# Kernel tuning notes

Hardware: AMD Instinct MI355X
Metric: run time of the kernel (lower is better)

## Reference

```python
import jax, jax.numpy as jnp
import numpy as np

B, T, H, S = 2, 2048, 16, 64
E = H * S  # 1024

def layernorm(x, w, b, eps=1e-5):
    mu = jnp.mean(x, axis=-1, keepdims=True)
    var = jnp.mean((x - mu) ** 2, axis=-1, keepdims=True)
    return (x - mu) * jax.lax.rsqrt(var + eps) * w + b

def setup_inputs() -> dict:
    key = jax.random.key(0)
    ks = jax.random.split(key, 12)
    w = lambda k, shape: (0.02 * jax.random.normal(k, shape)).astype(jnp.float32)
    return {
        "x": jax.random.normal(ks[0], (B, T, E), dtype=jnp.float32),
        "prev": jax.random.normal(ks[1], (B, T, T, H), dtype=jnp.float32),
        "kqv_w": w(ks[2], (3 * S, S)),      # torch Linear weight [out,in], no bias
        "proj_w": w(ks[3], (E, E)),
        "ln1_w": jnp.ones((E,), jnp.float32),
        "ln1_b": jnp.zeros((E,), jnp.float32),
        "ln2_w": jnp.ones((E,), jnp.float32),
        "ln2_b": jnp.zeros((E,), jnp.float32),
        "ff_w1": w(ks[4], (4 * E, E)),
        "ff_b1": jnp.zeros((4 * E,), jnp.float32),
        "ff_w2": w(ks[5], (E, 4 * E)),
        "ff_b2": jnp.zeros((E,), jnp.float32),
    }

def reference(x, prev, kqv_w, proj_w, ln1_w, ln1_b, ln2_w, ln2_b, ff_w1, ff_b1, ff_w2, ff_b2):
    b, t, _ = x.shape
    xh = x.reshape(b, t, H, S)                       # [B,T,H,S]
    kqv = jnp.einsum('bths,os->btho', xh, kqv_w)     # [B,T,H,3S]
    k, q, v = jnp.split(kqv, 3, axis=-1)             # split order: k,q,v
    att_score = jnp.einsum('bihk,bjhk->bijh', q, k) / jnp.sqrt(jnp.float32(S)) + prev
    att = jax.nn.softmax(att_score, axis=2)          # softmax over j (keys)
    res = jnp.einsum('btih,bihs->bths', att, v).reshape(b, t, E)
    mha = res @ proj_w.T                             # proj, dropout=0
    x1 = layernorm(x + mha, ln1_w, ln1_b)
    ff = jax.nn.gelu(x1 @ ff_w1.T + ff_b1, approximate=False) @ ff_w2.T + ff_b2
    x2 = layernorm(x1 + ff, ln2_w, ln2_b)
    return x2, att_score
```

## Files before the change

kernel.cpp:

```cpp
#include <hip/hip_runtime.h>
#include <hip/hip_bf16.h>
#include <math.h>

#define Bd 2
#define Td 2048
#define Hd 16
#define Sd 64
#define Ed 1024
#define Fd 4096

typedef __attribute__((ext_vector_type(8))) short short8;
typedef __attribute__((ext_vector_type(4))) float f32x4;
typedef __hip_bfloat16 bf16;

__device__ __forceinline__ unsigned short f2bfu(float f){
  bf16 h = __float2bfloat16(f);
  unsigned short u;
  __builtin_memcpy(&u, &h, 2);
  return u;
}

__global__ __launch_bounds__(256) void cvt_bf16_kernel(const float* __restrict__ src,
                                                       bf16* __restrict__ dst, int n4){
  int i = blockIdx.x*256 + threadIdx.x;
  int stride = gridDim.x*256;
  for (; i < n4; i += stride){
    float4 v = ((const float4*)src)[i];
    bf16* d = dst + (size_t)i*4;
    d[0] = __float2bfloat16(v.x);
    d[1] = __float2bfloat16(v.y);
    d[2] = __float2bfloat16(v.z);
    d[3] = __float2bfloat16(v.w);
  }
}

__global__ __launch_bounds__(192) void kqv_kernel(const float* __restrict__ x, const float* __restrict__ w,
    bf16* __restrict__ kb, bf16* __restrict__ qb, bf16* __restrict__ vb){
  __shared__ float xs[Ed];
  int bt = blockIdx.x;
  int o = threadIdx.x;
  const float* xrow = x + (size_t)bt*Ed;
  for (int i = o; i < Ed; i += 192) xs[i] = xrow[i];
  __syncthreads();
  float4 wr[16];
  const float4* w4 = (const float4*)(w + o*Sd);
  #pragma unroll
  for (int i = 0; i < 16; i++) wr[i] = w4[i];
  int part = o >> 6, sidx = o & 63;
  bf16* ob = (part == 0) ? kb : (part == 1 ? qb : vb);
  ob += (size_t)bt*Hd*Sd + sidx;
  for (int h = 0; h < Hd; h++){
    const float4* xh4 = (const float4*)(xs + h*Sd);
    float a0=0.f,a1=0.f,a2=0.f,a3=0.f;
    #pragma unroll
    for (int i = 0; i < 16; i++){
      float4 xv = xh4[i];
      a0 = fmaf(xv.x, wr[i].x, a0);
      a1 = fmaf(xv.y, wr[i].y, a1);
      a2 = fmaf(xv.z, wr[i].z, a2);
      a3 = fmaf(xv.w, wr[i].w, a3);
    }
    ob[h*Sd] = __float2bfloat16((a0+a1)+(a2+a3));
  }
}

__global__ __launch_bounds__(256) void vt_kernel(const bf16* __restrict__ vb, bf16* __restrict__ vt){
  __shared__ bf16 tile[64][72];
  int t0 = blockIdx.x*64, h = blockIdx.y, b = blockIdx.z;
  int tid = threadIdx.x;
  for (int i = tid; i < 4096; i += 256){
    int tt = i >> 6, s = i & 63;
    tile[tt][s] = vb[(((size_t)b*Td + t0 + tt)*Hd + h)*Sd + s];
  }
  __syncthreads();
  for (int i = tid; i < 4096; i += 256){
    int s = i >> 6, tt = i & 63;
    vt[(((size_t)b*Hd + h)*Sd + s)*Td + t0 + tt] = tile[tt][s];
  }
}

__global__ __launch_bounds__(1024) void attn_score_kernel(
    const bf16* __restrict__ qb, const bf16* __restrict__ kb,
    const float* __restrict__ prev, float* __restrict__ att,
    float* __restrict__ m_ws, float* __restrict__ linv_ws){
  int i0 = blockIdx.x*16, b = blockIdx.y;
  int tid = threadIdx.x;
  int wid = tid >> 6, lane = tid & 63, col = lane & 15, quad = lane >> 4;
  __shared__ float Ss[16][16][17];
  __shared__ float Mp[4][16][16];
  __shared__ float Lp[4][16][16];

  const bf16* qbase = qb + (((size_t)b*Td + i0 + col)*Hd + wid)*Sd + quad*8;
  short8 aq0 = *(const short8*)(qbase);
  short8 aq1 = *(const short8*)(qbase + 32);

  int ii = tid >> 6, jq = (tid >> 4) & 3, h2 = tid & 15;
  float m_t = -1e30f, l_t = 0.f;

  for (int jt = 0; jt < Td/16; jt++){
    int j0 = jt*16;
    const bf16* kbase = kb + (((size_t)b*Td + j0 + col)*Hd + wid)*Sd + quad*8;
    short8 bk0 = *(const short8*)(kbase);
    short8 bk1 = *(const short8*)(kbase + 32);
    f32x4 acc = {0.f, 0.f, 0.f, 0.f};
    acc = __builtin_amdgcn_mfma_f32_16x16x32_bf16(aq0, bk0, acc, 0, 0, 0);
    acc = __builtin_amdgcn_mfma_f32_16x16x32_bf16(aq1, bk1, acc, 0, 0, 0);
    #pragma unroll
    for (int r = 0; r < 4; r++) Ss[wid][quad*4 + r][col] = acc[r];
    __syncthreads();
    {
      size_t gb = (((size_t)b*Td + i0 + ii)*Td + j0 + jq*4)*Hd + h2;
      float v0 = Ss[h2][ii][jq*4+0]*0.125f + prev[gb];
      float v1 = Ss[h2][ii][jq*4+1]*0.125f + prev[gb + Hd];
      float v2 = Ss[h2][ii][jq*4+2]*0.125f + prev[gb + 2*Hd];
      float v3 = Ss[h2][ii][jq*4+3]*0.125f + prev[gb + 3*Hd];
      att[gb]        = v0;
      att[gb + Hd]   = v1;
      att[gb + 2*Hd] = v2;
      att[gb + 3*Hd] = v3;
      float mx = fmaxf(fmaxf(v0, v1), fmaxf(v2, v3));
      float nm = fmaxf(m_t, mx);
      float sc = __expf(m_t - nm);
      l_t = l_t*sc + __expf(v0-nm) + __expf(v1-nm) + __expf(v2-nm) + __expf(v3-nm);
      m_t = nm;
    }
    __syncthreads();
  }
  Mp[jq][ii][h2] = m_t;
  Lp[jq][ii][h2] = l_t;
  __syncthreads();
  if (jq == 0){
    float m0 = Mp[0][ii][h2], m1 = Mp[1][ii][h2], m2 = Mp[2][ii][h2], m3 = Mp[3][ii][h2];
    float M = fmaxf(fmaxf(m0, m1), fmaxf(m2, m3));
    float L = Lp[0][ii][h2]*__expf(m0-M) + Lp[1][ii][h2]*__expf(m1-M)
            + Lp[2][ii][h2]*__expf(m2-M) + Lp[3][ii][h2]*__expf(m3-M);
    size_t sidx = ((size_t)b*Td + i0 + ii)*Hd + h2;
    m_ws[sidx] = M;
    linv_ws[sidx] = 1.0f / L;
  }
}

__global__ __launch_bounds__(1024) void attn_av_kernel(
    const float* __restrict__ att, const bf16* __restrict__ vt,
    const float* __restrict__ m_ws, const float* __restrict__ linv_ws,
    bf16* __restrict__ resb){
  int i0 = blockIdx.x*16, b = blockIdx.y;
  int tid = threadIdx.x;
  int wid = tid >> 6, lane = tid & 63, col = lane & 15, quad = lane >> 4;
  __shared__ __align__(16) bf16 Ps[16][17][40];
  __shared__ float Msh[16][16], Lsh[16][16];
  if (tid < 256){
    int ri = tid >> 4, rh = tid & 15;
    size_t sidx = ((size_t)b*Td + i0 + ri)*Hd + rh;
    Msh[ri][rh] = m_ws[sidx];
    Lsh[ri][rh] = linv_ws[sidx];
  }
  __syncthreads();
  f32x4 O[4];
  #pragma unroll
  for (int st = 0; st < 4; st++) O[st] = (f32x4){0.f,0.f,0.f,0.f};

  int cii = tid >> 6, co = (tid >> 4) & 3, ch = tid & 15;
  float mrow = Msh[cii][ch];
  const bf16* vbase = vt + (((size_t)b*Hd + wid)*Sd + col)*Td;

  for (int jt = 0; jt < Td/32; jt++){
    int j0 = jt*32;
    size_t gb = (((size_t)b*Td + i0 + cii)*Td + j0 + co*8)*Hd + ch;
    short8 sv;
    #pragma unroll
    for (int e = 0; e < 8; e++){
      sv[e] = (short)f2bfu(__expf(att[gb + (size_t)e*Hd] - mrow));
    }
    *(short8*)(&Ps[ch][cii][co*8]) = sv;
    __syncthreads();
    short8 a = *(const short8*)(&Ps[wid][col][quad*8]);
    #pragma unroll
    for (int st = 0; st < 4; st++){
      short8 bv = *(const short8*)(vbase + (size_t)st*16*Td + j0 + quad*8);
      O[st] = __builtin_amdgcn_mfma_f32_16x16x32_bf16(a, bv, O[st], 0, 0, 0);
    }
    __syncthreads();
  }
  #pragma unroll
  for (int st = 0; st < 4; st++){
    #pragma unroll
    for (int r = 0; r < 4; r++){
      int irow = quad*4 + r;
      float val = O[st][r] * Lsh[irow][wid];
      resb[((size_t)b*Td + i0 + irow)*Ed + wid*Sd + st*16 + col] = __float2bfloat16(val);
    }
  }
}

template<int EPI>
__global__ __launch_bounds__(256) void gemm_kernel(
    const bf16* __restrict__ A, const bf16* __restrict__ Bw,
    int M, int N, int K,
    const float* __restrict__ bias, const float* __restrict__ addend,
    float* __restrict__ outf, bf16* __restrict__ outb){
  __shared__ __align__(16) bf16 As[128*32];
  __shared__ __align__(16) bf16 Bs[128*32];
  int tid = threadIdx.x;
  int wid = tid >> 6, lane = tid & 63, col = lane & 15, quad = lane >> 4;
  int n0 = blockIdx.x*128, m0 = blockIdx.y*128;
  int wy = wid >> 1, wx = wid & 1;
  f32x4 acc[4][4];
  #pragma unroll
  for (int i = 0; i < 4; i++)
    #pragma unroll
    for (int j = 0; j < 4; j++) acc[i][j] = (f32x4){0.f,0.f,0.f,0.f};

  int srow = tid >> 2, skc = tid & 3;
  for (int k0 = 0; k0 < K; k0 += 32){
    __syncthreads();
    #pragma unroll
    for (int i = 0; i < 2; i++){
      const bf16* gpa = A + (size_t)(m0 + srow + i*64)*K + k0 + skc*8;
      bf16* lpa = As + ((size_t)i*256 + wid*64)*8;
      __builtin_amdgcn_global_load_lds((const __attribute__((address_space(1))) unsigned int*)gpa,
                                       (__attribute__((address_space(3))) unsigned int*)lpa, 16, 0, 0);
      const bf16* gpb = Bw + (size_t)(n0 + srow + i*64)*K + k0 + skc*8;
      bf16* lpb = Bs + ((size_t)i*256 + wid*64)*8;
      __builtin_amdgcn_global_load_lds((const __attribute__((address_space(1))) unsigned int*)gpb,
                                       (__attribute__((address_space(3))) unsigned int*)lpb, 16, 0, 0);
    }
    __syncthreads();
    short8 af[4], bf_[4];
    #pragma unroll
    for (int t = 0; t < 4; t++){
      af[t]  = *(const short8*)(As + (wy*64 + t*16 + col)*32 + quad*8);
      bf_[t] = *(const short8*)(Bs + (wx*64 + t*16 + col)*32 + quad*8);
    }
    #pragma unroll
    for (int i = 0; i < 4; i++)
      #pragma unroll
      for (int j = 0; j < 4; j++)
        acc[i][j] = __builtin_amdgcn_mfma_f32_16x16x32_bf16(af[i], bf_[j], acc[i][j], 0, 0, 0);
  }
  #pragma unroll
  for (int i = 0; i < 4; i++){
    #pragma unroll
    for (int r = 0; r < 4; r++){
      int mrow = m0 + wy*64 + i*16 + quad*4 + r;
      #pragma unroll
      for (int j = 0; j < 4; j++){
        int ncol = n0 + wx*64 + j*16 + col;
        float v = acc[i][j][r];
        size_t oidx = (size_t)mrow*N + ncol;
        if (EPI == 0){
          outf[oidx] = v + addend[oidx];
        } else if (EPI == 1){
          float t = v + bias[ncol];
          outb[oidx] = __float2bfloat16(0.5f*t*(1.0f + erff(t*0.70710678118f)));
        } else {
          outf[oidx] = v + bias[ncol] + addend[oidx];
        }
      }
    }
  }
}

__global__ __launch_bounds__(256) void ln_kernel(const float* __restrict__ in,
    const float* __restrict__ gw, const float* __restrict__ gb,
    float* __restrict__ outf, bf16* __restrict__ outb){
  int row = blockIdx.x, tid = threadIdx.x;
  const float4* r4 = (const float4*)(in + (size_t)row*Ed);
  float4 xv = r4[tid];
  float s  = xv.x + xv.y + xv.z + xv.w;
  float ss = xv.x*xv.x + xv.y*xv.y + xv.z*xv.z + xv.w*xv.w;
  #pragma unroll
  for (int off = 32; off > 0; off >>= 1){
    s  += __shfl_down(s, off);
    ss += __shfl_down(ss, off);
  }
  __shared__ float sb[4], ssb[4], mv[2];
  int lane = tid & 63, wv = tid >> 6;
  if (lane == 0){ sb[wv] = s; ssb[wv] = ss; }
  __syncthreads();
  if (tid == 0){
    float S  = sb[0]+sb[1]+sb[2]+sb[3];
    float SS = ssb[0]+ssb[1]+ssb[2]+ssb[3];
    float mean = S*(1.0f/Ed);
    float var  = SS*(1.0f/Ed) - mean*mean;
    mv[0] = mean; mv[1] = rsqrtf(var + 1e-5f);
  }
  __syncthreads();
  float mean = mv[0], rstd = mv[1];
  float4 wv4 = ((const float4*)gw)[tid];
  float4 bv4 = ((const float4*)gb)[tid];
  float4 o;
  o.x = (xv.x - mean)*rstd*wv4.x + bv4.x;
  o.y = (xv.y - mean)*rstd*wv4.y + bv4.y;
  o.z = (xv.z - mean)*rstd*wv4.z + bv4.z;
  o.w = (xv.w - mean)*rstd*wv4.w + bv4.w;
  if (outf) ((float4*)(outf + (size_t)row*Ed))[tid] = o;
  if (outb){
    bf16* ob = outb + (size_t)row*Ed + tid*4;
    ob[0] = __float2bfloat16(o.x);
    ob[1] = __float2bfloat16(o.y);
    ob[2] = __float2bfloat16(o.z);
    ob[3] = __float2bfloat16(o.w);
  }
}

extern "C" void kernel_launch(void* const* d_in, const int* in_sizes, int n_in,
                              void* d_out, int out_size, void* d_ws, size_t ws_size,
                              hipStream_t stream){
  (void)in_sizes; (void)n_in; (void)out_size; (void)ws_size;
  const float* x      = (const float*)d_in[0];
  const float* prev   = (const float*)d_in[1];
  const float* kqv_w  = (const float*)d_in[2];
  const float* proj_w = (const float*)d_in[3];
  const float* ln1_w  = (const float*)d_in[4];
  const float* ln1_b  = (const float*)d_in[5];
  const float* ln2_w  = (const float*)d_in[6];
  const float* ln2_b  = (const float*)d_in[7];
  const float* ff_w1  = (const float*)d_in[8];
  const float* ff_b1  = (const float*)d_in[9];
  const float* ff_w2  = (const float*)d_in[10];
  const float* ff_b2  = (const float*)d_in[11];

  float* out_x2  = (float*)d_out;
  float* out_att = out_x2 + (size_t)Bd*Td*Ed;

  char* wsp = (char*)d_ws;
  auto alloc = [&](size_t bytes)->char*{
    char* p = wsp;
    wsp += (bytes + 255) & ~(size_t)255;
    return p;
  };
  const size_t NTOK = (size_t)Bd*Td;
  bf16* kb    = (bf16*)alloc(NTOK*Ed*2);
  bf16* qb    = (bf16*)alloc(NTOK*Ed*2);
  bf16* vb    = (bf16*)alloc(NTOK*Ed*2);
  bf16* vtb   = (bf16*)alloc(NTOK*Ed*2);
  bf16* resb  = (bf16*)alloc(NTOK*Ed*2);
  bf16* x1b   = (bf16*)alloc(NTOK*Ed*2);
  bf16* hidb  = (bf16*)alloc(NTOK*Fd*2);
  bf16* pwb   = (bf16*)alloc((size_t)Ed*Ed*2);
  bf16* w1b   = (bf16*)alloc((size_t)Fd*Ed*2);
  bf16* w2b   = (bf16*)alloc((size_t)Ed*Fd*2);
  float* m_ws    = (float*)alloc(NTOK*Hd*4);
  float* linv_ws = (float*)alloc(NTOK*Hd*4);
  float* sum_ws  = (float*)alloc(NTOK*Ed*4);
  float* x1f     = (float*)alloc(NTOK*Ed*4);

  cvt_bf16_kernel<<<1024, 256, 0, stream>>>(proj_w, pwb, (Ed*Ed)/4);
  cvt_bf16_kernel<<<4096, 256, 0, stream>>>(ff_w1, w1b, (Fd*Ed)/4);
  cvt_bf16_kernel<<<4096, 256, 0, stream>>>(ff_w2, w2b, (Ed*Fd)/4);

  kqv_kernel<<<Bd*Td, 192, 0, stream>>>(x, kqv_w, kb, qb, vb);
  vt_kernel<<<dim3(Td/64, Hd, Bd), 256, 0, stream>>>(vb, vtb);

  attn_score_kernel<<<dim3(Td/16, Bd), 1024, 0, stream>>>(qb, kb, prev, out_att, m_ws, linv_ws);
  attn_av_kernel<<<dim3(Td/16, Bd), 1024, 0, stream>>>(out_att, vtb, m_ws, linv_ws, resb);

  gemm_kernel<0><<<dim3(Ed/128, (Bd*Td)/128), 256, 0, stream>>>(
      resb, pwb, Bd*Td, Ed, Ed, nullptr, x, sum_ws, nullptr);
  ln_kernel<<<Bd*Td, 256, 0, stream>>>(sum_ws, ln1_w, ln1_b, x1f, x1b);
  gemm_kernel<1><<<dim3(Fd/128, (Bd*Td)/128), 256, 0, stream>>>(
      x1b, w1b, Bd*Td, Fd, Ed, ff_b1, nullptr, nullptr, hidb);
  gemm_kernel<2><<<dim3(Ed/128, (Bd*Td)/128), 256, 0, stream>>>(
      hidb, w2b, Bd*Td, Ed, Fd, ff_b2, x1f, sum_ws, nullptr);
  ln_kernel<<<Bd*Td, 256, 0, stream>>>(sum_ws, ln2_w, ln2_b, out_x2, nullptr);
}
```

Before: 1.727 ms.

## Fuse attention score and AV kernels into one online-softmax pass

Merges the score kernel and the AV kernel into one kernel that computes scores, writes att_score, and accumulates P·V with an online softmax that rescales the output accumulators. This removes the second full read of the large att tensor from global memory and the m/linv workspace round trip. It also prefetches the next K and prev tiles, processes 32 keys per iteration, and replaces __syncthreads with a custom LDS-wait barrier. In exchange it uses more registers and does extra rescaling work in every iteration.

```diff
diff --git a/kernel.cpp b/kernel.cpp
--- a/kernel.cpp
+++ b/kernel.cpp
@@ -18,6 +18,12 @@
   unsigned short u;
   __builtin_memcpy(&u, &h, 2);
   return u;
+}
+
+__device__ __forceinline__ void bar_lds(){
+  asm volatile("s_waitcnt lgkmcnt(0)" ::: "memory");
+  __builtin_amdgcn_s_barrier();
+  asm volatile("" ::: "memory");
 }
 
 __global__ __launch_bounds__(256) void cvt_bf16_kernel(const float* __restrict__ src,
@@ -79,117 +85,134 @@
   }
 }
 
-__global__ __launch_bounds__(1024) void attn_score_kernel(
+__global__ __launch_bounds__(1024) void attn_fused_kernel(
     const bf16* __restrict__ qb, const bf16* __restrict__ kb,
-    const float* __restrict__ prev, float* __restrict__ att,
-    float* __restrict__ m_ws, float* __restrict__ linv_ws){
+    const bf16* __restrict__ vtp, const float* __restrict__ prev,
+    float* __restrict__ att, bf16* __restrict__ resb){
+  constexpr int NT = Td/32;
   int i0 = blockIdx.x*16, b = blockIdx.y;
   int tid = threadIdx.x;
   int wid = tid >> 6, lane = tid & 63, col = lane & 15, quad = lane >> 4;
-  __shared__ float Ss[16][16][17];
-  __shared__ float Mp[4][16][16];
-  __shared__ float Lp[4][16][16];
+  __shared__ float Ss[16][17][33];
+  __shared__ __align__(16) bf16 Ps[16][17][40];
+  __shared__ float Msc[16][16];
+  __shared__ float Linv[16][16];
 
   const bf16* qbase = qb + (((size_t)b*Td + i0 + col)*Hd + wid)*Sd + quad*8;
   short8 aq0 = *(const short8*)(qbase);
   short8 aq1 = *(const short8*)(qbase + 32);
 
-  int ii = tid >> 6, jq = (tid >> 4) & 3, h2 = tid & 15;
+  int ii = wid, co = (tid >> 4) & 3, h2 = tid & 15;
   float m_t = -1e30f, l_t = 0.f;
 
-  for (int jt = 0; jt < Td/16; jt++){
-    int j0 = jt*16;
-    const bf16* kbase = kb + (((size_t)b*Td + j0 + col)*Hd + wid)*Sd + quad*8;
-    short8 bk0 = *(const short8*)(kbase);
-    short8 bk1 = *(const short8*)(kbase + 32);
-    f32x4 acc = {0.f, 0.f, 0.f, 0.f};
-    acc = __builtin_amdgcn_mfma_f32_16x16x32_bf16(aq0, bk0, acc, 0, 0, 0);
-    acc = __builtin_amdgcn_mfma_f32_16x16x32_bf16(aq1, bk1, acc, 0, 0, 0);
-    #pragma unroll
-    for (int r = 0; r < 4; r++) Ss[wid][quad*4 + r][col] = acc[r];
-    __syncthreads();
+  const bf16* vbase = vtp + (((size_t)b*Hd + wid)*Sd + col)*Td;
+  const bf16* kb0 = kb + (((size_t)b*Td + col)*Hd + wid)*Sd + quad*8;
+  const size_t KJ = (size_t)Hd*Sd;
+
+  short8 kc0 = *(const short8*)(kb0);
+  short8 kc1 = *(const short8*)(kb0 + 32);
+  short8 kc2 = *(const short8*)(kb0 + 16*KJ);
+  short8 kc3 = *(const short8*)(kb0 + 16*KJ + 32);
+
+  const size_t pbase = (((size_t)b*Td + i0 + ii)*Td)*(size_t)Hd + h2;
+  float pf[8];
+  #pragma unroll
+  for (int e = 0; e < 8; e++) pf[e] = prev[pbase + (size_t)(co*8 + e)*Hd];
+
+  f32x4 O0 = {0.f,0.f,0.f,0.f}, O1 = O0, O2 = O0, O3 = O0;
+
+#define PV_TILE(JP) do { \
+    float s0 = Msc[quad*4+0][wid]; \
+    float s1 = Msc[quad*4+1][wid]; \
+    float s2 = Msc[quad*4+2][wid]; \
+    float s3 = Msc[quad*4+3][wid]; \
+    O0[0]*=s0; O0[1]*=s1; O0[2]*=s2; O0[3]*=s3; \
+    O1[0]*=s0; O1[1]*=s1; O1[2]*=s2; O1[3]*=s3; \
+    O2[0]*=s0; O2[1]*=s1; O2[2]*=s2; O2[3]*=s3; \
+    O3[0]*=s0; O3[1]*=s1; O3[2]*=s2; O3[3]*=s3; \
+    short8 ap  = *(const short8*)(&Ps[wid][col][quad*8]); \
+    short8 bv0 = *(const short8*)(vbase + (JP) + quad*8); \
+    short8 bv1 = *(const short8*)(vbase + (size_t)16*Td + (JP) + quad*8); \
+    short8 bv2 = *(const short8*)(vbase + (size_t)32*Td + (JP) + quad*8); \
+    short8 bv3 = *(const short8*)(vbase + (size_t)48*Td + (JP) + quad*8); \
+    O0 = __builtin_amdgcn_mfma_f32_16x16x32_bf16(ap, bv0, O0, 0, 0, 0); \
+    O1 = __builtin_amdgcn_mfma_f32_16x16x32_bf16(ap, bv1, O1, 0, 0, 0); \
+    O2 = __builtin_amdgcn_mfma_f32_16x16x32_bf16(ap, bv2, O2, 0, 0, 0); \
+    O3 = __builtin_amdgcn_mfma_f32_16x16x32_bf16(ap, bv3, O3, 0, 0, 0); \
+  } while (0)
+
+  for (int jt = 0; jt < NT; jt++){
+    int j0 = jt*32;
+    if (jt > 0){
+      PV_TILE(j0 - 32);
+    }
+    f32x4 acc0 = {0.f,0.f,0.f,0.f}, acc1 = acc0;
+    acc0 = __builtin_amdgcn_mfma_f32_16x16x32_bf16(aq0, kc0, acc0, 0, 0, 0);
+    acc0 = __builtin_amdgcn_mfma_f32_16x16x32_bf16(aq1, kc1, acc0, 0, 0, 0);
+    acc1 = __builtin_amdgcn_mfma_f32_16x16x32_bf16(aq0, kc2, acc1, 0, 0, 0);
+    acc1 = __builtin_amdgcn_mfma_f32_16x16x32_bf16(aq1, kc3, acc1, 0, 0, 0);
     {
-      size_t gb = (((size_t)b*Td + i0 + ii)*Td + j0 + jq*4)*Hd + h2;
-      float v0 = Ss[h2][ii][jq*4+0]*0.125f + prev[gb];
-      float v1 = Ss[h2][ii][jq*4+1]*0.125f + prev[gb + Hd];
-      float v2 = Ss[h2][ii][jq*4+2]*0.125f + prev[gb + 2*Hd];
-      float v3 = Ss[h2][ii][jq*4+3]*0.125f + prev[gb + 3*Hd];
-      att[gb]        = v0;
-      att[gb + Hd]   = v1;
-      att[gb + 2*Hd] = v2;
-      att[gb + 3*Hd] = v3;
-      float mx = fmaxf(fmaxf(v0, v1), fmaxf(v2, v3));
-      float nm = fmaxf(m_t, mx);
-      float sc = __expf(m_t - nm);
-      l_t = l_t*sc + __expf(v0-nm) + __expf(v1-nm) + __expf(v2-nm) + __expf(v3-nm);
-      m_t = nm;
-    }
-    __syncthreads();
-  }
-  Mp[jq][ii][h2] = m_t;
-  Lp[jq][ii][h2] = l_t;
-  __syncthreads();
-  if (jq == 0){
-    float m0 = Mp[0][ii][h2], m1 = Mp[1][ii][h2], m2 = Mp[2][ii][h2], m3 = Mp[3][ii][h2];
-    float M = fmaxf(fmaxf(m0, m1), fmaxf(m2, m3));
-    float L = Lp[0][ii][h2]*__expf(m0-M) + Lp[1][ii][h2]*__expf(m1-M)
-            + Lp[2][ii][h2]*__expf(m2-M) + Lp[3][ii][h2]*__expf(m3-M);
-    size_t sidx = ((size_t)b*Td + i0 + ii)*Hd + h2;
-    m_ws[sidx] = M;
-    linv_ws[sidx] = 1.0f / L;
-  }
-}
-
-__global__ __launch_bounds__(1024) void attn_av_kernel(
-    const float* __restrict__ att, const bf16* __restrict__ vt,
-    const float* __restrict__ m_ws, const float* __restrict__ linv_ws,
-    bf16* __restrict__ resb){
-  int i0 = blockIdx.x*16, b = blockIdx.y;
-  int tid = threadIdx.x;
-  int wid = tid >> 6, lane = tid & 63, col = lane & 15, quad = lane >> 4;
-  __shared__ __align__(16) bf16 Ps[16][17][40];
-  __shared__ float Msh[16][16], Lsh[16][16];
-  if (tid < 256){
-    int ri = tid >> 4, rh = tid & 15;
-    size_t sidx = ((size_t)b*Td + i0 + ri)*Hd + rh;
-    Msh[ri][rh] = m_ws[sidx];
-    Lsh[ri][rh] = linv_ws[sidx];
-  }
-  __syncthreads();
-  f32x4 O[4];
-  #pragma unroll
-  for (int st = 0; st < 4; st++) O[st] = (f32x4){0.f,0.f,0.f,0.f};
-
-  int cii = tid >> 6, co = (tid >> 4) & 3, ch = tid & 15;
-  float mrow = Msh[cii][ch];
-  const bf16* vbase = vt + (((size_t)b*Hd + wid)*Sd + col)*Td;
-
-  for (int jt = 0; jt < Td/32; jt++){
-    int j0 = jt*32;
-    size_t gb = (((size_t)b*Td + i0 + cii)*Td + j0 + co*8)*Hd + ch;
+      int jn = (jt+1 < NT) ? (j0+32) : 0;
+      const bf16* knb = kb0 + (size_t)jn*KJ;
+      kc0 = *(const short8*)(knb);
+      kc1 = *(const short8*)(knb + 32);
+      kc2 = *(const short8*)(knb + 16*KJ);
+      kc3 = *(const short8*)(knb + 16*KJ + 32);
+    }
+    #pragma unroll
+    for (int r = 0; r < 4; r++){
+      Ss[wid][quad*4+r][col]      = acc0[r];
+      Ss[wid][quad*4+r][16 + col] = acc1[r];
+    }
+    bar_lds();
+    float v[8];
+    #pragma unroll
+    for (int e = 0; e < 8; e++) v[e] = Ss[h2][ii][co*8+e]*0.125f + pf[e];
+    {
+      int jn = (jt+1 < NT) ? (j0+32) : j0;
+      #pragma unroll
+      for (int e = 0; e < 8; e++) pf[e] = prev[pbase + (size_t)(jn + co*8 + e)*Hd];
+    }
+    size_t gb = pbase + (size_t)(j0 + co*8)*Hd;
+    #pragma unroll
+    for (int e = 0; e < 8; e++) att[gb + (size_t)e*Hd] = v[e];
+    float mx = fmaxf(fmaxf(fmaxf(v[0],v[1]), fmaxf(v[2],v[3])),
+                     fmaxf(fmaxf(v[4],v[5]), fmaxf(v[6],v[7])));
+    mx = fmaxf(mx, __shfl_xor(mx, 16));
+    mx = fmaxf(mx, __shfl_xor(mx, 32));
+    float m_new = fmaxf(m_t, mx);
+    float sc = __expf(m_t - m_new);
+    float p[8]; float ps = 0.f;
+    #pragma unroll
+    for (int e = 0; e < 8; e++){ p[e] = __expf(v[e] - m_new); ps += p[e]; }
+    l_t = l_t*sc + ps;
+    m_t = m_new;
+    if (co == 0) Msc[ii][h2] = sc;
     short8 sv;
     #pragma unroll
-    for (int e = 0; e < 8; e++){
-      sv[e] = (short)f2bfu(__expf(att[gb + (size_t)e*Hd] - mrow));
-    }
-    *(short8*)(&Ps[ch][cii][co*8]) = sv;
-    __syncthreads();
-    short8 a = *(const short8*)(&Ps[wid][col][quad*8]);
-    #pragma unroll
-    for (int st = 0; st < 4; st++){
-      short8 bv = *(const short8*)(vbase + (size_t)st*16*Td + j0 + quad*8);
-      O[st] = __builtin_amdgcn_mfma_f32_16x16x32_bf16(a, bv, O[st], 0, 0, 0);
-    }
-    __syncthreads();
-  }
-  #pragma unroll
-  for (int st = 0; st < 4; st++){
-    #pragma unroll
-    for (int r = 0; r < 4; r++){
-      int irow = quad*4 + r;
-      float val = O[st][r] * Lsh[irow][wid];
-      resb[((size_t)b*Td + i0 + irow)*Ed + wid*Sd + st*16 + col] = __float2bfloat16(val);
-    }
+    for (int e = 0; e < 8; e++) sv[e] = (short)f2bfu(p[e]);
+    *(short8*)(&Ps[h2][ii][co*8]) = sv;
+    bar_lds();
+  }
+  PV_TILE(Td - 32);
+#undef PV_TILE
+
+  float lsum = l_t + __shfl_xor(l_t, 16);
+  lsum += __shfl_xor(lsum, 32);
+  if (co == 0) Linv[ii][h2] = 1.0f / lsum;
+  bar_lds();
+  float li0 = Linv[quad*4+0][wid];
+  float li1 = Linv[quad*4+1][wid];
+  float li2 = Linv[quad*4+2][wid];
+  float li3 = Linv[quad*4+3][wid];
+  #pragma unroll
+  for (int r = 0; r < 4; r++){
+    float li = (r==0) ? li0 : (r==1) ? li1 : (r==2) ? li2 : li3;
+    size_t base = ((size_t)b*Td + i0 + quad*4 + r)*Ed + wid*Sd + col;
+    resb[base +  0] = __float2bfloat16(O0[r]*li);
+    resb[base + 16] = __float2bfloat16(O1[r]*li);
+    resb[base + 32] = __float2bfloat16(O2[r]*li);
+    resb[base + 48] = __float2bfloat16(O3[r]*li);
   }
 }
 
@@ -341,8 +364,6 @@
   bf16* pwb   = (bf16*)alloc((size_t)Ed*Ed*2);
   bf16* w1b   = (bf16*)alloc((size_t)Fd*Ed*2);
   bf16* w2b   = (bf16*)alloc((size_t)Ed*Fd*2);
-  float* m_ws    = (float*)alloc(NTOK*Hd*4);
-  float* linv_ws = (float*)alloc(NTOK*Hd*4);
   float* sum_ws  = (float*)alloc(NTOK*Ed*4);
   float* x1f     = (float*)alloc(NTOK*Ed*4);
 
@@ -353,8 +374,7 @@
   kqv_kernel<<<Bd*Td, 192, 0, stream>>>(x, kqv_w, kb, qb, vb);
   vt_kernel<<<dim3(Td/64, Hd, Bd), 256, 0, stream>>>(vb, vtb);
 
-  attn_score_kernel<<<dim3(Td/16, Bd), 1024, 0, stream>>>(qb, kb, prev, out_att, m_ws, linv_ws);
-  attn_av_kernel<<<dim3(Td/16, Bd), 1024, 0, stream>>>(out_att, vtb, m_ws, linv_ws, resb);
+  attn_fused_kernel<<<dim3(Td/16, Bd), 1024, 0, stream>>>(qb, kb, vtb, prev, out_att, resb);
 
   gemm_kernel<0><<<dim3(Ed/128, (Bd*Td)/128), 256, 0, stream>>>(
       resb, pwb, Bd*Td, Ed, Ed, nullptr, x, sum_ws, nullptr);
```

New measurement: 1.479 ms. 1.17x faster.
